# Performance work log

Hardware: AMD Instinct MI355X
Metric: run time of the kernel (lower is better)

The kernel has to match this reference:

```python
import jax, jax.numpy as jnp
import numpy as np

GROUP_SIZE = 32
OUT_FEATURES = 4096
IN_FEATURES = 4096


def _unpack_3bit(p):
    # p: [..., 3] uint8 -> [..., 8] 3-bit values in [0, 7]
    b0, b1, b2 = p[..., 0], p[..., 1], p[..., 2]
    v0 = b0 & 7
    v1 = (b0 >> 3) & 7
    v2 = ((b0 >> 6) & 3) | ((b1 & 1) << 2)
    v3 = (b1 >> 1) & 7
    v4 = (b1 >> 4) & 7
    v5 = ((b1 >> 7) & 1) | ((b2 & 3) << 1)
    v6 = (b2 >> 2) & 7
    v7 = (b2 >> 5) & 7
    return jnp.stack([v0, v1, v2, v3, v4, v5, v6, v7], axis=-1)


def _block_dequantize_3bit(packed, normalization, group_size=GROUP_SIZE):
    # packed: [n_groups, group_size*3//8] int8, normalization: [n_groups, 1]
    p = packed.astype(jnp.uint8).reshape(-1, group_size // 8, 3)
    q = _unpack_3bit(p).reshape(-1, group_size).astype(jnp.float32)
    n = normalization.astype(jnp.float32)  # [n_groups, 1]
    x_norm = q / 7.0
    return (x_norm * (2.0 * n) - n).reshape(-1)


def setup_inputs() -> dict:
    key = jax.random.key(0)
    k1, k2, k3, k4 = jax.random.split(key, 4)
    n_groups = OUT_FEATURES * IN_FEATURES // GROUP_SIZE
    packed_cols = GROUP_SIZE * 3 // 8
    x = jax.random.normal(k1, (2, 2048, IN_FEATURES), dtype=jnp.float32)
    weight_q3 = jax.random.randint(k2, (n_groups, packed_cols), 0, 256, dtype=jnp.int32).astype(jnp.int8)
    weight_norm = jax.random.uniform(k3, (n_groups, 1), dtype=jnp.float32, minval=0.05, maxval=1.0)
    bias = jax.random.normal(k4, (OUT_FEATURES,), dtype=jnp.float32) * 0.02
    return {"x": x, "weight_q3": weight_q3, "weight_norm": weight_norm, "bias": bias}


def reference(x, weight_q3, weight_norm, bias):
    # Dequantize 3-bit packed weights to fp32 [out, in], then F.linear.
    w = _block_dequantize_3bit(weight_q3, weight_norm).reshape(OUT_FEATURES, IN_FEATURES)
    return jnp.einsum('bsi,oi->bso', x, w) + bias
```

## Files before the change

### kernel.cpp

```cpp
#include <hip/hip_runtime.h>
#include <hip/hip_bf16.h>
#include <stdint.h>

#define OUTF 4096
#define INF  4096
#define MROWS 4096
#define GS 32

typedef __attribute__((ext_vector_type(8))) __bf16 bf16x8;
typedef __attribute__((ext_vector_type(4))) float f32x4;

__device__ inline void gload_lds16(const void* g, void* l) {
    __builtin_amdgcn_global_load_lds(
        (const __attribute__((address_space(1))) void*)g,
        (__attribute__((address_space(3))) void*)l, 16, 0, 0);
}

__global__ void cvt_x_kernel(const float* __restrict__ x, __bf16* __restrict__ xb, int n8) {
    int i = blockIdx.x * blockDim.x + threadIdx.x;
    if (i >= n8) return;
    const f32x4* xp = (const f32x4*)x;
    f32x4 a = xp[2 * i], b = xp[2 * i + 1];
    bf16x8 v = { (__bf16)a[0], (__bf16)a[1], (__bf16)a[2], (__bf16)a[3],
                 (__bf16)b[0], (__bf16)b[1], (__bf16)b[2], (__bf16)b[3] };
    ((bf16x8*)xb)[i] = v;
}

__device__ inline void load_group_bits(const int* __restrict__ wq, int gid,
                                       uint64_t& lo, uint64_t& hi) {
    const int4* p = (const int4*)(wq + (size_t)gid * 12);
    int4 A = p[0], B = p[1], C = p[2];
    uint32_t d0 = (uint32_t)(A.x & 255) | ((uint32_t)(A.y & 255) << 8) |
                  ((uint32_t)(A.z & 255) << 16) | ((uint32_t)(A.w & 255) << 24);
    uint32_t d1 = (uint32_t)(B.x & 255) | ((uint32_t)(B.y & 255) << 8) |
                  ((uint32_t)(B.z & 255) << 16) | ((uint32_t)(B.w & 255) << 24);
    uint32_t d2 = (uint32_t)(C.x & 255) | ((uint32_t)(C.y & 255) << 8) |
                  ((uint32_t)(C.z & 255) << 16) | ((uint32_t)(C.w & 255) << 24);
    lo = (uint64_t)d0 | ((uint64_t)d1 << 32);
    hi = (uint64_t)d1 | ((uint64_t)d2 << 32);
}

__global__ void dequant_w_kernel(const int* __restrict__ wq,
                                 const float* __restrict__ wn,
                                 __bf16* __restrict__ wb) {
    int gid = blockIdx.x * blockDim.x + threadIdx.x;
    uint64_t lo, hi;
    load_group_bits(wq, gid, lo, hi);
    float nrm = wn[gid];
    float c2 = nrm * (2.0f / 7.0f), c1 = -nrm;
    bf16x8 o[4];
#pragma unroll
    for (int j = 0; j < 32; ++j) {
        uint32_t q = (j <= 20) ? (uint32_t)((lo >> (3 * j)) & 7)
                               : (uint32_t)((hi >> (3 * j - 32)) & 7);
        o[j >> 3][j & 7] = (__bf16)((float)q * c2 + c1);
    }
    bf16x8* outp = (bf16x8*)(wb + (size_t)gid * 32);
    outp[0] = o[0]; outp[1] = o[1]; outp[2] = o[2]; outp[3] = o[3];
}


#define VMCNT(N) asm volatile("s_waitcnt vmcnt(" #N ")" ::: "memory")
#define BARR() do { asm volatile("" ::: "memory"); __builtin_amdgcn_s_barrier(); \
                    asm volatile("" ::: "memory"); } while (0)

#define LOADA(RB, H) do { \
    _Pragma("unroll") \
    for (int m_ = 0; m_ < 4; ++m_) { \
        const int r_ = wr * 64 + m_ * 16 + row16; \
        _Pragma("unroll") \
        for (int kk_ = 0; kk_ < 2; ++kk_) \
            af[m_][kk_] = *(const bf16x8*)(lds + (RB) * 65536 + (H) * 16384 + \
                r_ * 128 + (((kk_ * 4 + kq) * 16) ^ ((r_ & 7) << 4))); \
    } \
} while (0)

#define LOADB(RB, H) do { \
    _Pragma("unroll") \
    for (int n_ = 0; n_ < 2; ++n_) { \
        const int r_ = wc * 32 + n_ * 16 + row16; \
        _Pragma("unroll") \
        for (int kk_ = 0; kk_ < 2; ++kk_) \
            bf[n_][kk_] = *(const bf16x8*)(lds + (RB) * 65536 + 32768 + (H) * 16384 + \
                r_ * 128 + (((kk_ * 4 + kq) * 16) ^ ((r_ & 7) << 4))); \
    } \
} while (0)

#define STAGEA(SB, H, SKT) do { \
    _Pragma("unroll") \
    for (int j_ = 0; j_ < 2; ++j_) \
        gload_lds16((const char*)(xb + (size_t)(bm * 256 + (H) * 128 + j_ * 64 + srow) * INF + \
                                  (SKT) * 64 + schunk * 8), \
                    lds + (SB) * 65536 + (H) * 16384 + j_ * 8192 + tid * 16); \
} while (0)

#define STAGEB(SB, H, SKT) do { \
    _Pragma("unroll") \
    for (int j_ = 0; j_ < 2; ++j_) \
        gload_lds16((const char*)(wb + (size_t)(bn * 256 + (H) * 128 + j_ * 64 + srow) * INF + \
                                  (SKT) * 64 + schunk * 8), \
                    lds + (SB) * 65536 + 32768 + (H) * 16384 + j_ * 8192 + tid * 16); \
} while (0)

#define MFMA16(MH, NH) do { \
    __builtin_amdgcn_s_setprio(1); \
    _Pragma("unroll") \
    for (int kk_ = 0; kk_ < 2; ++kk_) \
        _Pragma("unroll") \
        for (int m_ = 0; m_ < 4; ++m_) \
            _Pragma("unroll") \
            for (int n_ = 0; n_ < 2; ++n_) \
                acc[MH][NH][m_][n_] = __builtin_amdgcn_mfma_f32_16x16x32_bf16( \
                    af[m_][kk_], bf[n_][kk_], acc[MH][NH][m_][n_], 0, 0, 0); \
    __builtin_amdgcn_s_setprio(0); \
} while (0)

#define HALF_ITER(RB, SB, SKT) do { \
    LOADA(RB, 0); LOADB(RB, 0); STAGEA(SB, 0, SKT); VMCNT(2); BARR(); MFMA16(0, 0); BARR(); \
    LOADB(RB, 1);               STAGEB(SB, 0, SKT);           BARR(); MFMA16(0, 1); BARR(); \
    LOADA(RB, 1);               STAGEA(SB, 1, SKT);           BARR(); MFMA16(1, 1); BARR(); \
    LOADB(RB, 0);               STAGEB(SB, 1, SKT); VMCNT(4); BARR(); MFMA16(1, 0); BARR(); \
} while (0)

__global__ __launch_bounds__(512, 2) void gemm8_kernel(
    const __bf16* __restrict__ xb, const __bf16* __restrict__ wb,
    const float* __restrict__ bias, float* __restrict__ out) {
    __shared__ __align__(16) unsigned char lds[131072];

    const int tid = threadIdx.x;
    const int lane = tid & 63, wid = tid >> 6;
    const int wr = wid >> 2, wc = wid & 3;
    const int row16 = lane & 15, kq = lane >> 4;

    const int bid = blockIdx.x;
    const int wg = (bid & 7) * 32 + (bid >> 3);
    const int bn = wg & 15, bm = wg >> 4;

    const int srow = tid >> 3;
    const int schunk = (tid & 7) ^ (srow & 7);

    f32x4 acc[2][2][4][2] = {};
    bf16x8 af[4][2], bf[2][2];

    STAGEA(0, 0, 0); STAGEB(0, 0, 0); STAGEA(0, 1, 0); STAGEB(0, 1, 0);
    VMCNT(4);
    BARR();

    for (int kt = 0; kt < INF / 64; kt += 2) {
        const int s1 = kt + 1;
        const int s2 = (kt + 2) & 63;
        HALF_ITER(0, 1, s1);
        HALF_ITER(1, 0, s2);
    }

#pragma unroll
    for (int nh = 0; nh < 2; ++nh)
#pragma unroll
        for (int n = 0; n < 2; ++n) {
            const int col = bn * 256 + nh * 128 + wc * 32 + n * 16 + row16;
            const float bv = bias[col];
#pragma unroll
            for (int mh = 0; mh < 2; ++mh)
#pragma unroll
                for (int m = 0; m < 4; ++m) {
                    const int rbase = bm * 256 + mh * 128 + wr * 64 + m * 16 + kq * 4;
#pragma unroll
                    for (int j = 0; j < 4; ++j)
                        out[(size_t)(rbase + j) * OUTF + col] = acc[mh][nh][m][n][j] + bv;
                }
        }
}

__global__ __launch_bounds__(256, 2) void gemm_fb_kernel(
    const float* __restrict__ x, const int* __restrict__ wq,
    const float* __restrict__ wn, const float* __restrict__ bias,
    float* __restrict__ out) {
    __shared__ __align__(16) unsigned char lAraw[128 * 128];
    __shared__ __align__(16) unsigned char lBraw[128 * 128];

    const int tid = threadIdx.x;
    const int lane = tid & 63, wid = tid >> 6;
    const int wr = wid >> 1, wc = wid & 1;
    const int bn = blockIdx.x, bm = blockIdx.y;
    const int row16 = lane & 15, kq = lane >> 4;

    f32x4 acc[4][4] = {};

    int aoff[4], boff[4];
#pragma unroll
    for (int m = 0; m < 4; ++m) {
        int r = wr * 64 + m * 16 + row16;
        aoff[m] = r * 128 + ((kq * 16) ^ ((r & 7) << 4));
    }
#pragma unroll
    for (int n = 0; n < 4; ++n) {
        int r = wc * 64 + n * 16 + row16;
        boff[n] = r * 128 + ((kq * 16) ^ ((r & 7) << 4));
    }

    for (int kt = 0; kt < INF / 64; ++kt) {
        __syncthreads();
#pragma unroll
        for (int it = 0; it < 4; ++it) {
            int row = it * 32 + (tid >> 3), c = tid & 7;
            const f32x4* xp = (const f32x4*)(x + (size_t)(bm * 128 + row) * INF + kt * 64 + c * 8);
            f32x4 a0 = xp[0], a1 = xp[1];
            bf16x8 v = { (__bf16)a0[0], (__bf16)a0[1], (__bf16)a0[2], (__bf16)a0[3],
                         (__bf16)a1[0], (__bf16)a1[1], (__bf16)a1[2], (__bf16)a1[3] };
            *(bf16x8*)(lAraw + row * 128 + ((c * 16) ^ ((row & 7) << 4))) = v;
        }
        {
            int row = tid >> 1, gi = tid & 1;
            int gid = (bn * 128 + row) * (INF / GS) + kt * 2 + gi;
            uint64_t lo, hi;
            load_group_bits(wq, gid, lo, hi);
            float nrm = wn[gid];
            float c2 = nrm * (2.0f / 7.0f), c1 = -nrm;
            bf16x8 o[4];
#pragma unroll
            for (int j = 0; j < 32; ++j) {
                uint32_t q = (j <= 20) ? (uint32_t)((lo >> (3 * j)) & 7)
                                       : (uint32_t)((hi >> (3 * j - 32)) & 7);
                o[j >> 3][j & 7] = (__bf16)((float)q * c2 + c1);
            }
            unsigned swz = (row & 7) << 4;
#pragma unroll
            for (int c4 = 0; c4 < 4; ++c4)
                *(bf16x8*)(lBraw + row * 128 + ((gi * 64 + c4 * 16) ^ swz)) = o[c4];
        }
        __syncthreads();

#pragma unroll
        for (int kk = 0; kk < 2; ++kk) {
            bf16x8 afr[4], bfr[4];
#pragma unroll
            for (int m = 0; m < 4; ++m)
                afr[m] = *(const bf16x8*)(lAraw + (aoff[m] ^ (kk * 64)));
#pragma unroll
            for (int n = 0; n < 4; ++n)
                bfr[n] = *(const bf16x8*)(lBraw + (boff[n] ^ (kk * 64)));
#pragma unroll
            for (int m = 0; m < 4; ++m)
#pragma unroll
                for (int n = 0; n < 4; ++n)
                    acc[m][n] = __builtin_amdgcn_mfma_f32_16x16x32_bf16(afr[m], bfr[n], acc[m][n], 0, 0, 0);
        }
    }

#pragma unroll
    for (int n = 0; n < 4; ++n) {
        int col = bn * 128 + wc * 64 + n * 16 + row16;
        float bv = bias[col];
#pragma unroll
        for (int m = 0; m < 4; ++m) {
            int rbase = bm * 128 + wr * 64 + m * 16 + kq * 4;
#pragma unroll
            for (int j = 0; j < 4; ++j)
                out[(size_t)(rbase + j) * OUTF + col] = acc[m][n][j] + bv;
        }
    }
}

extern "C" void kernel_launch(void* const* d_in, const int* in_sizes, int n_in,
                              void* d_out, int out_size, void* d_ws, size_t ws_size,
                              hipStream_t stream) {
    const float* x    = (const float*)d_in[0];
    const int*   wq   = (const int*)d_in[1];
    const float* wn   = (const float*)d_in[2];
    const float* bias = (const float*)d_in[3];
    float* out = (float*)d_out;

    const size_t xb_bytes = (size_t)MROWS * INF * 2;
    const size_t wb_bytes = (size_t)OUTF * INF * 2;
    if (ws_size >= xb_bytes + wb_bytes) {
        __bf16* xb = (__bf16*)d_ws;
        __bf16* wb = (__bf16*)((char*)d_ws + xb_bytes);
        cvt_x_kernel<<<(MROWS * INF / 8 + 255) / 256, 256, 0, stream>>>(x, xb, MROWS * INF / 8);
        dequant_w_kernel<<<(OUTF * INF / GS) / 256, 256, 0, stream>>>(wq, wn, wb);
        gemm8_kernel<<<(MROWS / 256) * (OUTF / 256), 512, 0, stream>>>(xb, wb, bias, out);
    } else {
        gemm_fb_kernel<<<dim3(OUTF / 128, MROWS / 128), 256, 0, stream>>>(x, wq, wn, bias, out);
    }
}
```

Baseline: 142.4 us.

## Switch main GEMM to 32x32x16 MFMA and deepen LDS staging pipeline

Replaces the 16x16x32 bf16 MFMA tiles with 32x32x16 MFMA instructions, restructuring LDS fragment loads, accumulators and the output write mapping to match. The staging schedule also changes: the B half for the next tile is issued earlier into the other buffer, giving an extra stage of prefetch with a looser vmcnt wait. The larger MFMA shape cuts the instruction count and the number of LDS reads per flop. It also changes register pressure and makes the buffer-reuse ordering more delicate.

Measured after the change: 165.8 us. 16.4% more time.

```diff
diff --git a/kernel.cpp b/kernel.cpp
--- a/kernel.cpp
+++ b/kernel.cpp
@@ -9,6 +9,7 @@
 
 typedef __attribute__((ext_vector_type(8))) __bf16 bf16x8;
 typedef __attribute__((ext_vector_type(4))) float f32x4;
+typedef __attribute__((ext_vector_type(16))) float f32x16;
 
 __device__ inline void gload_lds16(const void* g, void* l) {
     __builtin_amdgcn_global_load_lds(
@@ -66,60 +67,53 @@
 
 #define LOADA(RB, H) do { \
     _Pragma("unroll") \
-    for (int m_ = 0; m_ < 4; ++m_) { \
-        const int r_ = wr * 64 + m_ * 16 + row16; \
+    for (int mb_ = 0; mb_ < 2; ++mb_) { \
+        const int r_ = wr * 64 + mb_ * 32 + l31; \
         _Pragma("unroll") \
-        for (int kk_ = 0; kk_ < 2; ++kk_) \
-            af[m_][kk_] = *(const bf16x8*)(lds + (RB) * 65536 + (H) * 16384 + \
-                r_ * 128 + (((kk_ * 4 + kq) * 16) ^ ((r_ & 7) << 4))); \
+        for (int ks_ = 0; ks_ < 4; ++ks_) \
+            af[mb_][ks_] = *(const bf16x8*)(lds + (RB) * 65536 + (H) * 16384 + \
+                r_ * 128 + (((ks_ * 2 + l5) * 16) ^ ((r_ & 7) << 4))); \
     } \
 } while (0)
 
 #define LOADB(RB, H) do { \
-    _Pragma("unroll") \
-    for (int n_ = 0; n_ < 2; ++n_) { \
-        const int r_ = wc * 32 + n_ * 16 + row16; \
+    const int r_ = wc * 32 + l31; \
+    _Pragma("unroll") \
+    for (int ks_ = 0; ks_ < 4; ++ks_) \
+        bf[ks_] = *(const bf16x8*)(lds + (RB) * 65536 + 32768 + (H) * 16384 + \
+            r_ * 128 + (((ks_ * 2 + l5) * 16) ^ ((r_ & 7) << 4))); \
+} while (0)
+
+#define STAGE(SB, AB, H, SKT) do { \
+    const __bf16* base_ = (AB) ? wb : xb; \
+    const int brc_ = ((AB) ? bn : bm) * 256; \
+    _Pragma("unroll") \
+    for (int j_ = 0; j_ < 2; ++j_) \
+        gload_lds16((const char*)(base_ + (size_t)(brc_ + (H) * 128 + j_ * 64 + srow) * INF + \
+                                  (SKT) * 64 + schunk * 8), \
+                    lds + (SB) * 65536 + (AB) * 32768 + (H) * 16384 + j_ * 8192 + tid * 16); \
+} while (0)
+
+#define MFMA_Q(MH, NH) do { \
+    __builtin_amdgcn_s_setprio(1); \
+    _Pragma("unroll") \
+    for (int ks_ = 0; ks_ < 4; ++ks_) \
         _Pragma("unroll") \
-        for (int kk_ = 0; kk_ < 2; ++kk_) \
-            bf[n_][kk_] = *(const bf16x8*)(lds + (RB) * 65536 + 32768 + (H) * 16384 + \
-                r_ * 128 + (((kk_ * 4 + kq) * 16) ^ ((r_ & 7) << 4))); \
-    } \
-} while (0)
-
-#define STAGEA(SB, H, SKT) do { \
-    _Pragma("unroll") \
-    for (int j_ = 0; j_ < 2; ++j_) \
-        gload_lds16((const char*)(xb + (size_t)(bm * 256 + (H) * 128 + j_ * 64 + srow) * INF + \
-                                  (SKT) * 64 + schunk * 8), \
-                    lds + (SB) * 65536 + (H) * 16384 + j_ * 8192 + tid * 16); \
-} while (0)
-
-#define STAGEB(SB, H, SKT) do { \
-    _Pragma("unroll") \
-    for (int j_ = 0; j_ < 2; ++j_) \
-        gload_lds16((const char*)(wb + (size_t)(bn * 256 + (H) * 128 + j_ * 64 + srow) * INF + \
-                                  (SKT) * 64 + schunk * 8), \
-                    lds + (SB) * 65536 + 32768 + (H) * 16384 + j_ * 8192 + tid * 16); \
-} while (0)
-
-#define MFMA16(MH, NH) do { \
-    __builtin_amdgcn_s_setprio(1); \
-    _Pragma("unroll") \
-    for (int kk_ = 0; kk_ < 2; ++kk_) \
-        _Pragma("unroll") \
-        for (int m_ = 0; m_ < 4; ++m_) \
-            _Pragma("unroll") \
-            for (int n_ = 0; n_ < 2; ++n_) \
-                acc[MH][NH][m_][n_] = __builtin_amdgcn_mfma_f32_16x16x32_bf16( \
-                    af[m_][kk_], bf[n_][kk_], acc[MH][NH][m_][n_], 0, 0, 0); \
+        for (int mb_ = 0; mb_ < 2; ++mb_) \
+            acc[MH][NH][mb_] = __builtin_amdgcn_mfma_f32_32x32x16_bf16( \
+                af[mb_][ks_], bf[ks_], acc[MH][NH][mb_], 0, 0, 0); \
     __builtin_amdgcn_s_setprio(0); \
 } while (0)
 
-#define HALF_ITER(RB, SB, SKT) do { \
-    LOADA(RB, 0); LOADB(RB, 0); STAGEA(SB, 0, SKT); VMCNT(2); BARR(); MFMA16(0, 0); BARR(); \
-    LOADB(RB, 1);               STAGEB(SB, 0, SKT);           BARR(); MFMA16(0, 1); BARR(); \
-    LOADA(RB, 1);               STAGEA(SB, 1, SKT);           BARR(); MFMA16(1, 1); BARR(); \
-    LOADB(RB, 0);               STAGEB(SB, 1, SKT); VMCNT(4); BARR(); MFMA16(1, 0); BARR(); \
+#define TILE(RB, T) do { \
+    LOADA(RB, 0); LOADB(RB, 0); STAGE((RB) ^ 1, 1, 0, ((T) + 1) & 63); \
+        BARR(); MFMA_Q(0, 0); BARR(); \
+    LOADB(RB, 1); STAGE(RB, 0, 0, ((T) + 2) & 63); \
+        BARR(); MFMA_Q(0, 1); BARR(); \
+    LOADA(RB, 1); STAGE(RB, 1, 1, ((T) + 2) & 63); \
+        BARR(); MFMA_Q(1, 1); BARR(); \
+    LOADB(RB, 0); STAGE(RB, 0, 1, ((T) + 2) & 63); VMCNT(6); \
+        BARR(); MFMA_Q(1, 0); BARR(); \
 } while (0)
 
 __global__ __launch_bounds__(512, 2) void gemm8_kernel(
@@ -130,7 +124,7 @@
     const int tid = threadIdx.x;
     const int lane = tid & 63, wid = tid >> 6;
     const int wr = wid >> 2, wc = wid & 3;
-    const int row16 = lane & 15, kq = lane >> 4;
+    const int l31 = lane & 31, l5 = lane >> 5;
 
     const int bid = blockIdx.x;
     const int wg = (bid & 7) * 32 + (bid >> 3);
@@ -139,36 +133,35 @@
     const int srow = tid >> 3;
     const int schunk = (tid & 7) ^ (srow & 7);
 
-    f32x4 acc[2][2][4][2] = {};
-    bf16x8 af[4][2], bf[2][2];
-
-    STAGEA(0, 0, 0); STAGEB(0, 0, 0); STAGEA(0, 1, 0); STAGEB(0, 1, 0);
-    VMCNT(4);
+    f32x16 acc[2][2][2] = {};
+    bf16x8 af[2][4], bf[4];
+
+    STAGE(0, 0, 0, 0); STAGE(0, 1, 0, 0); STAGE(0, 1, 1, 0); STAGE(0, 0, 1, 0);
+    STAGE(1, 0, 0, 1); STAGE(1, 1, 1, 1); STAGE(1, 0, 1, 1);
+    VMCNT(6);
     BARR();
 
     for (int kt = 0; kt < INF / 64; kt += 2) {
-        const int s1 = kt + 1;
-        const int s2 = (kt + 2) & 63;
-        HALF_ITER(0, 1, s1);
-        HALF_ITER(1, 0, s2);
-    }
-
-#pragma unroll
-    for (int nh = 0; nh < 2; ++nh)
-#pragma unroll
-        for (int n = 0; n < 2; ++n) {
-            const int col = bn * 256 + nh * 128 + wc * 32 + n * 16 + row16;
-            const float bv = bias[col];
-#pragma unroll
-            for (int mh = 0; mh < 2; ++mh)
-#pragma unroll
-                for (int m = 0; m < 4; ++m) {
-                    const int rbase = bm * 256 + mh * 128 + wr * 64 + m * 16 + kq * 4;
-#pragma unroll
-                    for (int j = 0; j < 4; ++j)
-                        out[(size_t)(rbase + j) * OUTF + col] = acc[mh][nh][m][n][j] + bv;
+        TILE(0, kt);
+        TILE(1, kt + 1);
+    }
+
+#pragma unroll
+    for (int nh = 0; nh < 2; ++nh) {
+        const int col = bn * 256 + nh * 128 + wc * 32 + l31;
+        const float bv = bias[col];
+#pragma unroll
+        for (int mh = 0; mh < 2; ++mh)
+#pragma unroll
+            for (int mb = 0; mb < 2; ++mb) {
+                const int rbase = bm * 256 + mh * 128 + wr * 64 + mb * 32 + 4 * l5;
+#pragma unroll
+                for (int r = 0; r < 16; ++r) {
+                    const int row = rbase + (r & 3) + 8 * (r >> 2);
+                    out[(size_t)row * OUTF + col] = acc[mh][nh][mb][r] + bv;
                 }
-        }
+            }
+    }
 }
 
 __global__ __launch_bounds__(256, 2) void gemm_fb_kernel(
```

## Simplify GEMM k-loop pipeline to one barrier per tile and merge prep kernels

Applied to the files above, without the earlier changes.

The GEMM main loop drops the eight-phase half-iteration schedule, with its explicit vmcnt waits and barriers around each MFMA quarter. In its place it issues all global-to-LDS staging for the next k-tile up front, double-buffers the B fragments in registers, and uses a single __syncthreads per tile. The aim is fewer barriers and waits, letting LDS reads overlap MFMA work. The trade-off is that the tuned interleaving of staging and compute is lost, and __syncthreads drains all outstanding loads. Separately, the x-to-bf16 conversion and weight dequantization kernels are merged into one launch to save a kernel launch and its tail.

Result: slower. 145.8 us (+2.4%).

```diff
diff --git a/kernel.cpp b/kernel.cpp
--- a/kernel.cpp
+++ b/kernel.cpp
@@ -14,16 +14,6 @@
     __builtin_amdgcn_global_load_lds(
         (const __attribute__((address_space(1))) void*)g,
         (__attribute__((address_space(3))) void*)l, 16, 0, 0);
-}
-
-__global__ void cvt_x_kernel(const float* __restrict__ x, __bf16* __restrict__ xb, int n8) {
-    int i = blockIdx.x * blockDim.x + threadIdx.x;
-    if (i >= n8) return;
-    const f32x4* xp = (const f32x4*)x;
-    f32x4 a = xp[2 * i], b = xp[2 * i + 1];
-    bf16x8 v = { (__bf16)a[0], (__bf16)a[1], (__bf16)a[2], (__bf16)a[3],
-                 (__bf16)b[0], (__bf16)b[1], (__bf16)b[2], (__bf16)b[3] };
-    ((bf16x8*)xb)[i] = v;
 }
 
 __device__ inline void load_group_bits(const int* __restrict__ wq, int gid,
@@ -40,69 +30,69 @@
     hi = (uint64_t)d1 | ((uint64_t)d2 << 32);
 }
 
-__global__ void dequant_w_kernel(const int* __restrict__ wq,
-                                 const float* __restrict__ wn,
-                                 __bf16* __restrict__ wb) {
-    int gid = blockIdx.x * blockDim.x + threadIdx.x;
-    uint64_t lo, hi;
-    load_group_bits(wq, gid, lo, hi);
-    float nrm = wn[gid];
-    float c2 = nrm * (2.0f / 7.0f), c1 = -nrm;
-    bf16x8 o[4];
-#pragma unroll
-    for (int j = 0; j < 32; ++j) {
-        uint32_t q = (j <= 20) ? (uint32_t)((lo >> (3 * j)) & 7)
-                               : (uint32_t)((hi >> (3 * j - 32)) & 7);
-        o[j >> 3][j & 7] = (__bf16)((float)q * c2 + c1);
-    }
-    bf16x8* outp = (bf16x8*)(wb + (size_t)gid * 32);
-    outp[0] = o[0]; outp[1] = o[1]; outp[2] = o[2]; outp[3] = o[3];
-}
-
-
-#define VMCNT(N) asm volatile("s_waitcnt vmcnt(" #N ")" ::: "memory")
-#define BARR() do { asm volatile("" ::: "memory"); __builtin_amdgcn_s_barrier(); \
-                    asm volatile("" ::: "memory"); } while (0)
-
-#define LOADA(RB, H) do { \
+__global__ void prep_kernel(const float* __restrict__ x, __bf16* __restrict__ xb,
+                            const int* __restrict__ wq, const float* __restrict__ wn,
+                            __bf16* __restrict__ wb) {
+    const int bid = blockIdx.x;
+    if (bid < 8192) {
+        int i = bid * 256 + threadIdx.x;
+        const f32x4* xp = (const f32x4*)x;
+        f32x4 a = xp[2 * i], b = xp[2 * i + 1];
+        bf16x8 v = { (__bf16)a[0], (__bf16)a[1], (__bf16)a[2], (__bf16)a[3],
+                     (__bf16)b[0], (__bf16)b[1], (__bf16)b[2], (__bf16)b[3] };
+        ((bf16x8*)xb)[i] = v;
+    } else {
+        int gid = (bid - 8192) * 256 + threadIdx.x;
+        uint64_t lo, hi;
+        load_group_bits(wq, gid, lo, hi);
+        float nrm = wn[gid];
+        float c2 = nrm * (2.0f / 7.0f), c1 = -nrm;
+        bf16x8 o[4];
+#pragma unroll
+        for (int j = 0; j < 32; ++j) {
+            uint32_t q = (j <= 20) ? (uint32_t)((lo >> (3 * j)) & 7)
+                                   : (uint32_t)((hi >> (3 * j - 32)) & 7);
+            o[j >> 3][j & 7] = (__bf16)((float)q * c2 + c1);
+        }
+        bf16x8* outp = (bf16x8*)(wb + (size_t)gid * 32);
+        outp[0] = o[0]; outp[1] = o[1]; outp[2] = o[2]; outp[3] = o[3];
+    }
+}
+
+
+#define RD_A(DST, RB, H) do { \
     _Pragma("unroll") \
     for (int m_ = 0; m_ < 4; ++m_) { \
         const int r_ = wr * 64 + m_ * 16 + row16; \
         _Pragma("unroll") \
         for (int kk_ = 0; kk_ < 2; ++kk_) \
-            af[m_][kk_] = *(const bf16x8*)(lds + (RB) * 65536 + (H) * 16384 + \
+            DST[m_][kk_] = *(const bf16x8*)(lds + (RB) * 65536 + (H) * 16384 + \
                 r_ * 128 + (((kk_ * 4 + kq) * 16) ^ ((r_ & 7) << 4))); \
     } \
 } while (0)
 
-#define LOADB(RB, H) do { \
+#define RD_B(DST, RB, H) do { \
     _Pragma("unroll") \
     for (int n_ = 0; n_ < 2; ++n_) { \
         const int r_ = wc * 32 + n_ * 16 + row16; \
         _Pragma("unroll") \
         for (int kk_ = 0; kk_ < 2; ++kk_) \
-            bf[n_][kk_] = *(const bf16x8*)(lds + (RB) * 65536 + 32768 + (H) * 16384 + \
+            DST[n_][kk_] = *(const bf16x8*)(lds + (RB) * 65536 + 32768 + (H) * 16384 + \
                 r_ * 128 + (((kk_ * 4 + kq) * 16) ^ ((r_ & 7) << 4))); \
     } \
 } while (0)
 
-#define STAGEA(SB, H, SKT) do { \
+#define STAGE(SB, AB, H, SKT) do { \
+    const __bf16* base_ = (AB) ? wb : xb; \
+    const int brc_ = ((AB) ? bn : bm) * 256; \
     _Pragma("unroll") \
     for (int j_ = 0; j_ < 2; ++j_) \
-        gload_lds16((const char*)(xb + (size_t)(bm * 256 + (H) * 128 + j_ * 64 + srow) * INF + \
+        gload_lds16((const char*)(base_ + (size_t)(brc_ + (H) * 128 + j_ * 64 + srow) * INF + \
                                   (SKT) * 64 + schunk * 8), \
-                    lds + (SB) * 65536 + (H) * 16384 + j_ * 8192 + tid * 16); \
-} while (0)
-
-#define STAGEB(SB, H, SKT) do { \
-    _Pragma("unroll") \
-    for (int j_ = 0; j_ < 2; ++j_) \
-        gload_lds16((const char*)(wb + (size_t)(bn * 256 + (H) * 128 + j_ * 64 + srow) * INF + \
-                                  (SKT) * 64 + schunk * 8), \
-                    lds + (SB) * 65536 + 32768 + (H) * 16384 + j_ * 8192 + tid * 16); \
-} while (0)
-
-#define MFMA16(MH, NH) do { \
+                    lds + (SB) * 65536 + (AB) * 32768 + (H) * 16384 + j_ * 8192 + tid * 16); \
+} while (0)
+
+#define MF_Q(A_, B_, MH, NH) do { \
     __builtin_amdgcn_s_setprio(1); \
     _Pragma("unroll") \
     for (int kk_ = 0; kk_ < 2; ++kk_) \
@@ -111,15 +101,8 @@
             _Pragma("unroll") \
             for (int n_ = 0; n_ < 2; ++n_) \
                 acc[MH][NH][m_][n_] = __builtin_amdgcn_mfma_f32_16x16x32_bf16( \
-                    af[m_][kk_], bf[n_][kk_], acc[MH][NH][m_][n_], 0, 0, 0); \
+                    A_[m_][kk_], B_[n_][kk_], acc[MH][NH][m_][n_], 0, 0, 0); \
     __builtin_amdgcn_s_setprio(0); \
-} while (0)
-
-#define HALF_ITER(RB, SB, SKT) do { \
-    LOADA(RB, 0); LOADB(RB, 0); STAGEA(SB, 0, SKT); VMCNT(2); BARR(); MFMA16(0, 0); BARR(); \
-    LOADB(RB, 1);               STAGEB(SB, 0, SKT);           BARR(); MFMA16(0, 1); BARR(); \
-    LOADA(RB, 1);               STAGEA(SB, 1, SKT);           BARR(); MFMA16(1, 1); BARR(); \
-    LOADB(RB, 0);               STAGEB(SB, 1, SKT); VMCNT(4); BARR(); MFMA16(1, 0); BARR(); \
 } while (0)
 
 __global__ __launch_bounds__(512, 2) void gemm8_kernel(
@@ -140,17 +123,24 @@
     const int schunk = (tid & 7) ^ (srow & 7);
 
     f32x4 acc[2][2][4][2] = {};
-    bf16x8 af[4][2], bf[2][2];
-
-    STAGEA(0, 0, 0); STAGEB(0, 0, 0); STAGEA(0, 1, 0); STAGEB(0, 1, 0);
-    VMCNT(4);
-    BARR();
-
-    for (int kt = 0; kt < INF / 64; kt += 2) {
-        const int s1 = kt + 1;
-        const int s2 = (kt + 2) & 63;
-        HALF_ITER(0, 1, s1);
-        HALF_ITER(1, 0, s2);
+    bf16x8 a[4][2], b0[2][2], b1[2][2];
+
+    STAGE(0, 0, 0, 0); STAGE(0, 1, 0, 0); STAGE(0, 0, 1, 0); STAGE(0, 1, 1, 0);
+    __syncthreads();
+    RD_A(a, 0, 0); RD_B(b0, 0, 0);
+
+    for (int kt = 0; kt < INF / 64; ++kt) {
+        const int rb = kt & 1, sb = rb ^ 1, nt = (kt + 1) & 63;
+        STAGE(sb, 0, 0, nt); STAGE(sb, 1, 0, nt);
+        STAGE(sb, 0, 1, nt); STAGE(sb, 1, 1, nt);
+        RD_B(b1, rb, 1);
+        MF_Q(a, b0, 0, 0);
+        MF_Q(a, b1, 0, 1);
+        RD_A(a, rb, 1);
+        MF_Q(a, b1, 1, 1);
+        MF_Q(a, b0, 1, 0);
+        __syncthreads();
+        RD_A(a, sb, 0); RD_B(b0, sb, 0);
     }
 
 #pragma unroll
@@ -275,8 +265,7 @@
     if (ws_size >= xb_bytes + wb_bytes) {
         __bf16* xb = (__bf16*)d_ws;
         __bf16* wb = (__bf16*)((char*)d_ws + xb_bytes);
-        cvt_x_kernel<<<(MROWS * INF / 8 + 255) / 256, 256, 0, stream>>>(x, xb, MROWS * INF / 8);
-        dequant_w_kernel<<<(OUTF * INF / GS) / 256, 256, 0, stream>>>(wq, wn, wb);
+        prep_kernel<<<8192 + (OUTF * INF / GS) / 256, 256, 0, stream>>>(x, xb, wq, wn, wb);
         gemm8_kernel<<<(MROWS / 256) * (OUTF / 256), 512, 0, stream>>>(xb, wb, bias, out);
     } else {
         gemm_fb_kernel<<<dim3(OUTF / 128, MROWS / 128), 256, 0, stream>>>(x, wq, wn, bias, out);
```
